# Optimization experiments

Measured on AMD Instinct MI355X. Metric: run time of the kernel, lower is better.

Reference implementation:

```python
import jax, jax.numpy as jnp
import numpy as np

NUM_HEADS = 8


def setup_inputs() -> dict:
    key = jax.random.key(0)
    ks = jax.random.split(key, 8)
    B, N, D, H = 4, 1200, 256, NUM_HEADS
    return {
        "query_bbox": jax.random.normal(ks[0], (B, N, 10), jnp.float32) * 20.0,
        "query_feat": jax.random.normal(ks[1], (B, N, D), jnp.float32),
        "beta_w": jax.random.normal(ks[2], (H, D), jnp.float32) * 0.02,
        "beta_b": jax.random.uniform(ks[3], (H,), jnp.float32, 0.0, 2.0),
        "in_proj_w": jax.random.normal(ks[4], (3 * D, D), jnp.float32) * (D ** -0.5),
        "in_proj_b": jnp.zeros((3 * D,), jnp.float32),
        "out_proj_w": jax.random.normal(ks[5], (D, D), jnp.float32) * (D ** -0.5),
        "out_proj_b": jnp.zeros((D,), jnp.float32),
    }


def reference(query_bbox, query_feat, beta_w, beta_b, in_proj_w, in_proj_b,
              out_proj_w, out_proj_b):
    B, N, D = query_feat.shape
    H = NUM_HEADS
    hd = D // H

    # center_dists (no_grad in original): negative pairwise L2 of bbox centers
    centers = jax.lax.stop_gradient(query_bbox[..., :2])            # [B,N,2]
    diff = centers[:, :, None, :] - centers[:, None, :, :]          # [B,N,N,2]
    dist = -jnp.sqrt(jnp.sum(diff * diff, axis=-1))                 # [B,N,N]

    # per-head learned beta scale
    beta = jnp.einsum('bnd,hd->bhn', query_feat, beta_w) + beta_b[None, :, None]  # [B,H,N]
    attn_mask = dist[:, None, :, :] * beta[..., None]               # [B,H,N,N]

    # multi-head self-attention with additive mask
    qkv = jnp.einsum('bnd,ed->bne', query_feat, in_proj_w) + in_proj_b
    q, k, v = jnp.split(qkv, 3, axis=-1)
    q = q.reshape(B, N, H, hd)
    k = k.reshape(B, N, H, hd)
    v = v.reshape(B, N, H, hd)

    scores = jnp.einsum('bqhd,bkhd->bhqk', q, k) * (hd ** -0.5) + attn_mask
    attn = jax.nn.softmax(scores, axis=-1)                          # [B,H,N,N]
    out = jnp.einsum('bhqk,bkhd->bqhd', attn, v).reshape(B, N, D)
    return jnp.einsum('bnd,ed->bne', out, out_proj_w) + out_proj_b
```

## Files before the change

kernel.cpp:

```cpp
#include <hip/hip_runtime.h>
#include <hip/hip_bf16.h>

#define BC 4
#define NQ 1200
#define DIM 256
#define NH 8
#define HD 32
#define E3 768
#define MROWS (BC*NQ)
#define KPAD 1280
#define SCALE 0.17677669529663687f
#define L2E 1.4426950408889634f
#define SL2E (SCALE * L2E)

#define VT2_PER_BH 40960
#define VT2_PER_HH 20480

typedef __attribute__((ext_vector_type(8))) short bf16x8;
typedef __attribute__((ext_vector_type(4))) float f32x4;

__device__ inline short f2bf(float f) {
    __hip_bfloat16 h = __float2bfloat16(f);
    return *reinterpret_cast<short*>(&h);
}
__device__ inline unsigned pack2bf(float a, float b) {
    unsigned ua = (unsigned short)f2bf(a);
    unsigned ub = (unsigned short)f2bf(b);
    return ua | (ub << 16);
}

__global__ void beta_ctr_kernel(const float* __restrict__ feat, const float* __restrict__ bw,
                                const float* __restrict__ bb, const float* __restrict__ bbox,
                                float* __restrict__ beta, float* __restrict__ ctr) {
    int gw = (blockIdx.x * 256 + threadIdx.x) >> 6;
    int lane = threadIdx.x & 63;
    if (gw >= MROWS) return;
    const float* frow = feat + (size_t)gw * DIM;
    float acc[NH];
#pragma unroll
    for (int h = 0; h < NH; ++h) acc[h] = 0.f;
#pragma unroll
    for (int it = 0; it < DIM / 64; ++it) {
        int d = it * 64 + lane;
        float f = frow[d];
#pragma unroll
        for (int h = 0; h < NH; ++h) acc[h] += f * bw[h * DIM + d];
    }
#pragma unroll
    for (int h = 0; h < NH; ++h) {
#pragma unroll
        for (int off = 32; off; off >>= 1) acc[h] += __shfl_xor(acc[h], off);
    }
    int b = gw / NQ, n = gw % NQ;
#pragma unroll
    for (int h = 0; h < NH; ++h) {
        float v = acc[h] + bb[h];
        if (lane == h) beta[(b * NH + h) * NQ + n] = v;
    }
    if (lane == 0) {
        ctr[gw * 2]     = bbox[(size_t)gw * 10];
        ctr[gw * 2 + 1] = bbox[(size_t)gw * 10 + 1];
    }
}

template<bool AF32, bool BF32, bool OUTF32, bool VTOUT, bool QSCALE>
__global__ __launch_bounds__(256) void gemm_k256(const void* __restrict__ Av,
                                                 const void* __restrict__ Bv,
                                                 const float* __restrict__ bias,
                                                 void* __restrict__ Cout, int Edim,
                                                 short* __restrict__ vtout) {
    __shared__ short as[64][40];
    __shared__ short bs[64][40];
    int m0 = blockIdx.y * 64, e0 = blockIdx.x * 64;
    int t = threadIdx.x, lane = t & 63, wid = t >> 6;
    int wr = (wid >> 1) * 32, wc = (wid & 1) * 32;
    f32x4 acc[2][2] = {};
    int lrow = t >> 2, lch = t & 3;
    const float qs = (QSCALE && e0 < DIM) ? SL2E : 1.f;

    for (int ks = 0; ks < DIM / 32; ++ks) {
        bf16x8 av, wv;
        if (AF32) {
            const float* A = (const float*)Av;
            float4 f0 = *(const float4*)(A + (size_t)(m0 + lrow) * DIM + ks * 32 + lch * 8);
            float4 f1 = *(const float4*)(A + (size_t)(m0 + lrow) * DIM + ks * 32 + lch * 8 + 4);
            av[0]=f2bf(f0.x); av[1]=f2bf(f0.y); av[2]=f2bf(f0.z); av[3]=f2bf(f0.w);
            av[4]=f2bf(f1.x); av[5]=f2bf(f1.y); av[6]=f2bf(f1.z); av[7]=f2bf(f1.w);
        } else {
            av = *(const bf16x8*)((const short*)Av + (size_t)(m0 + lrow) * DIM + ks * 32 + lch * 8);
        }
        if (BF32) {
            const float* B = (const float*)Bv;
            float4 f0 = *(const float4*)(B + (size_t)(e0 + lrow) * DIM + ks * 32 + lch * 8);
            float4 f1 = *(const float4*)(B + (size_t)(e0 + lrow) * DIM + ks * 32 + lch * 8 + 4);
            wv[0]=f2bf(f0.x*qs); wv[1]=f2bf(f0.y*qs); wv[2]=f2bf(f0.z*qs); wv[3]=f2bf(f0.w*qs);
            wv[4]=f2bf(f1.x*qs); wv[5]=f2bf(f1.y*qs); wv[6]=f2bf(f1.z*qs); wv[7]=f2bf(f1.w*qs);
        } else {
            wv = *(const bf16x8*)((const short*)Bv + (size_t)(e0 + lrow) * DIM + ks * 32 + lch * 8);
        }
        __syncthreads();
        *(bf16x8*)&as[lrow][lch * 8] = av;
        *(bf16x8*)&bs[lrow][lch * 8] = wv;
        __syncthreads();
#pragma unroll
        for (int sm = 0; sm < 2; ++sm) {
            bf16x8 af = *(const bf16x8*)&as[wr + sm * 16 + (lane & 15)][(lane >> 4) * 8];
#pragma unroll
            for (int sn = 0; sn < 2; ++sn) {
                bf16x8 bfv = *(const bf16x8*)&bs[wc + sn * 16 + (lane & 15)][(lane >> 4) * 8];
                acc[sm][sn] = __builtin_amdgcn_mfma_f32_16x16x32_bf16(af, bfv, acc[sm][sn], 0, 0, 0);
            }
        }
    }
#pragma unroll
    for (int sm = 0; sm < 2; ++sm)
#pragma unroll
        for (int sn = 0; sn < 2; ++sn) {
            int e = e0 + wc + sn * 16 + (lane & 15);
            float bv = bias[e];
            if (QSCALE && e < DIM) bv *= SL2E;
            float vals[4];
            int mbase = m0 + wr + sm * 16 + (lane >> 4) * 4;
#pragma unroll
            for (int r = 0; r < 4; ++r) vals[r] = acc[sm][sn][r] + bv;
            if (VTOUT && e >= 2 * DIM) {
                int dv = e - 2 * DIM;
                int hv = dv >> 5, dd = dv & 31;
                int hh = dd >> 4, di = dd & 15;
                int bb = mbase / NQ, nn = mbase - bb * NQ;
                short4 o;
                o.x = f2bf(vals[0]); o.y = f2bf(vals[1]);
                o.z = f2bf(vals[2]); o.w = f2bf(vals[3]);
                size_t off = (size_t)(bb * NH + hv) * VT2_PER_BH + hh * VT2_PER_HH
                           + (nn >> 3) * 128 + di * 8 + (nn & 7);
                *(short4*)&vtout[off] = o;
            } else {
#pragma unroll
                for (int r = 0; r < 4; ++r) {
                    int m = mbase + r;
                    if (OUTF32) ((float*)Cout)[(size_t)m * Edim + e] = vals[r];
                    else        ((short*)Cout)[(size_t)m * Edim + e] = f2bf(vals[r]);
                }
            }
        }
}

#define KT_OFF 0
#define VT_OFF 8192
#define CK_OFF 16384
#define PL_OFF 17408
__global__ __launch_bounds__(256, 4) void attn_kernel(const short* __restrict__ qkv,
                                                      const short* __restrict__ vt2,
                                                      const float* __restrict__ beta,
                                                      const float* __restrict__ ctr,
                                                      short* __restrict__ attnb) {
    __shared__ __align__(16) char smem[25600];

    const int t = threadIdx.x, lane = t & 63, w = t >> 6;
    const int g = lane >> 4, i = lane & 15;
    const int qg = w >> 1, ksp = w & 1;
    const int bh = blockIdx.y, b = bh >> 3, h = bh & 7;
    const int q0 = blockIdx.x * 32 + qg * 16;
    const int q = q0 + i, qc = min(q, NQ - 1);
    const int kwb = ksp * 64;
    const int bq = b * NQ;

    bf16x8 qf = *(const bf16x8*)(qkv + (size_t)(bq + qc) * E3 + h * HD + g * 8);
    const float cqx = ctr[(bq + qc) * 2];
    const float cqy = ctr[(bq + qc) * 2 + 1];
    const float nbql = -beta[(b * NH + h) * NQ + qc] * L2E;

    float mcur = -1e30f, lsum = 0.f;
    f32x4 o0 = {}, o1 = {};

    const short* kgb = qkv + (size_t)bq * E3 + DIM + h * HD;
    const short* vgb = vt2 + (size_t)bh * VT2_PER_BH;
    const float* cgb = ctr + (size_t)bq * 2;

    bf16x8 sk0, sk1, sv0, sv1;
    float2 sc2;

    auto stage_load = [&](int kb) {
        int i0 = t, i1 = t + 256;
        int r0 = min(kb + ((i0 >> 6) << 4) + (i0 & 15), NQ - 1);
        int r1 = min(kb + ((i1 >> 6) << 4) + (i1 & 15), NQ - 1);
        sk0 = *(const bf16x8*)(kgb + (size_t)r0 * E3 + ((i0 >> 4) & 3) * 8);
        sk1 = *(const bf16x8*)(kgb + (size_t)r1 * E3 + ((i1 >> 4) & 3) * 8);
        sv0 = *(const bf16x8*)(vgb + (i0 >> 8) * VT2_PER_HH + ((kb >> 3) + ((i0 >> 4) & 15)) * 128 + (i0 & 15) * 8);
        sv1 = *(const bf16x8*)(vgb + (i1 >> 8) * VT2_PER_HH + ((kb >> 3) + ((i1 >> 4) & 15)) * 128 + (i1 & 15) * 8);
        if (t < 128) {
            int ky = min(kb + t, NQ - 1);
            sc2 = *(const float2*)(cgb + ky * 2);
        }
    };
    auto stage_write = [&]() {
        *(bf16x8*)&smem[KT_OFF + t * 16]         = sk0;
        *(bf16x8*)&smem[KT_OFF + (t + 256) * 16] = sk1;
        *(bf16x8*)&smem[VT_OFF + t * 16]         = sv0;
        *(bf16x8*)&smem[VT_OFF + (t + 256) * 16] = sv1;
        if (t < 128) *(float2*)&smem[CK_OFF + t * 8] = sc2;
    };

    stage_load(0);
    stage_write();
    __syncthreads();

    for (int kb = 0; kb < NQ; kb += 128) {
        const bool haveNext = (kb + 128 < NQ);
        const bool tail = (kb + 128 > NQ);
        if (haveNext) stage_load(kb + 128);

        float st[16];
#pragma unroll
        for (int kcl = 0; kcl < 4; ++kcl) {
            bf16x8 af = *(const bf16x8*)&smem[KT_OFF + ((((ksp * 4 + kcl) << 6) + lane) << 4)];
            f32x4 zero = {};
            f32x4 s = __builtin_amdgcn_mfma_f32_16x16x32_bf16(af, qf, zero, 0, 0, 0);
            int lk = kwb + kcl * 16 + 4 * g;
            float4 cA = *(const float4*)&smem[CK_OFF + lk * 8];
            float4 cB = *(const float4*)&smem[CK_OFF + lk * 8 + 16];
            float cxv[4] = {cA.x, cA.z, cB.x, cB.z};
            float cyv[4] = {cA.y, cA.w, cB.y, cB.w};
#pragma unroll
            for (int r = 0; r < 4; ++r) {
                float dx = cqx - cxv[r], dy = cqy - cyv[r];
                float d2 = __builtin_fmaf(dx, dx, dy * dy);
                float dist = __builtin_amdgcn_sqrtf(d2);
                st[kcl * 4 + r] = __builtin_fmaf(dist, nbql, s[r]);
            }
            if (tail) {
#pragma unroll
                for (int r = 0; r < 4; ++r)
                    if (kb + lk + r >= NQ) st[kcl * 4 + r] = -1e30f;
            }
        }

        float vm = st[0];
#pragma unroll
        for (int x = 1; x < 16; ++x) vm = fmaxf(vm, st[x]);
        vm = fmaxf(vm, __shfl_xor(vm, 16));
        vm = fmaxf(vm, __shfl_xor(vm, 32));
        if (!__all(vm <= mcur + 8.0f)) {
            float mnew = fmaxf(mcur, vm);
            float al = __builtin_amdgcn_exp2f(mcur - mnew);
            mcur = mnew;
            lsum *= al;
#pragma unroll
            for (int r = 0; r < 4; ++r) { o0[r] *= al; o1[r] *= al; }
        }
        float rs = 0.f;
#pragma unroll
        for (int x = 0; x < 16; ++x) {
            st[x] = __builtin_amdgcn_exp2f(st[x] - mcur);
            rs += st[x];
        }
        rs += __shfl_xor(rs, 16);
        rs += __shfl_xor(rs, 32);
        lsum += rs;

#pragma unroll
        for (int kcl = 0; kcl < 4; ++kcl) {
            int offb = PL_OFF + (((w << 10) + ((2 * kcl + (g >> 1)) << 7) + (i << 3) + ((g & 1) << 2)) << 1);
            *(unsigned*)&smem[offb]     = pack2bf(st[kcl * 4 + 0], st[kcl * 4 + 1]);
            *(unsigned*)&smem[offb + 4] = pack2bf(st[kcl * 4 + 2], st[kcl * 4 + 3]);
        }

#pragma unroll
        for (int kc2 = 0; kc2 < 2; ++kc2) {
            bf16x8 pbf = *(const bf16x8*)&smem[PL_OFF + (((w << 10) + ((kc2 * 4 + g) << 7) + (i << 3)) << 1)];
            int vidx = ((8 * ksp + 4 * kc2 + g) << 4) + i;
            bf16x8 vf0 = *(const bf16x8*)&smem[VT_OFF + (vidx << 4)];
            bf16x8 vf1 = *(const bf16x8*)&smem[VT_OFF + ((256 + vidx) << 4)];
            o0 = __builtin_amdgcn_mfma_f32_16x16x32_bf16(vf0, pbf, o0, 0, 0, 0);
            o1 = __builtin_amdgcn_mfma_f32_16x16x32_bf16(vf1, pbf, o1, 0, 0, 0);
        }

        if (haveNext) {
            __syncthreads();
            stage_write();
            __syncthreads();
        }
    }

    __syncthreads();
    float* mrg = (float*)smem;
    float* my = mrg + (w * 64 + lane) * 10;
    my[0] = mcur; my[1] = lsum;
#pragma unroll
    for (int r = 0; r < 4; ++r) { my[2 + r] = o0[r]; my[6 + r] = o1[r]; }
    __syncthreads();
    const float* pr = mrg + ((w ^ 1) * 64 + lane) * 10;
    float m2 = pr[0], l2 = pr[1];
    float mN = fmaxf(mcur, m2);
    float a1 = __builtin_amdgcn_exp2f(mcur - mN);
    float a2 = __builtin_amdgcn_exp2f(m2 - mN);
    float inv = 1.f / (lsum * a1 + l2 * a2);
    int hh = w & 1;
    f32x4 mine = hh ? o1 : o0;
    if (q < NQ) {
        short4 outv;
        float vals[4];
#pragma unroll
        for (int r = 0; r < 4; ++r) vals[r] = (mine[r] * a1 + pr[2 + hh * 4 + r] * a2) * inv;
        outv.x = f2bf(vals[0]); outv.y = f2bf(vals[1]);
        outv.z = f2bf(vals[2]); outv.w = f2bf(vals[3]);
        *(short4*)&attnb[(size_t)(bq + q) * DIM + h * HD + hh * 16 + 4 * g] = outv;
    }
}

extern "C" void kernel_launch(void* const* d_in, const int* in_sizes, int n_in,
                              void* d_out, int out_size, void* d_ws, size_t ws_size,
                              hipStream_t stream) {
    const float* bbox  = (const float*)d_in[0];
    const float* feat  = (const float*)d_in[1];
    const float* bw    = (const float*)d_in[2];
    const float* bb    = (const float*)d_in[3];
    const float* in_w  = (const float*)d_in[4];
    const float* in_b  = (const float*)d_in[5];
    const float* out_w = (const float*)d_in[6];
    const float* out_b = (const float*)d_in[7];
    float* out = (float*)d_out;

    char* ws = (char*)d_ws;
    size_t off = 0;
    auto alloc = [&](size_t bytes) { void* p = ws + off; off += (bytes + 255) & ~255ull; return p; };
    short* qkvb  = (short*)alloc((size_t)MROWS * E3 * 2);
    short* vtb   = (short*)alloc((size_t)BC * NH * VT2_PER_BH * 2);
    short* attnb = (short*)alloc((size_t)MROWS * DIM * 2);
    float* betab = (float*)alloc((size_t)BC * NH * NQ * 4);
    float* ctr   = (float*)alloc((size_t)BC * NQ * 2 * 4 + 1024);
    (void)ws_size; (void)in_sizes; (void)n_in; (void)out_size;

    beta_ctr_kernel<<<MROWS / 4, 256, 0, stream>>>(feat, bw, bb, bbox, betab, ctr);
    gemm_k256<true, true, false, true, true><<<dim3(E3 / 64, MROWS / 64), 256, 0, stream>>>(feat, in_w, in_b, qkvb, E3, vtb);
    attn_kernel<<<dim3((NQ + 31) / 32, BC * NH), 256, 0, stream>>>(qkvb, vtb, betab, ctr, attnb);
    gemm_k256<false, true, true, false, false><<<dim3(DIM / 64, MROWS / 64), 256, 0, stream>>>(attnb, out_w, out_b, out, DIM, nullptr);
}
```

Baseline: 59.96 us.

## Split each attention block's key range across four waves with 16 queries per block

The attention kernel now handles 16 queries per block instead of 32, and the four waves split each 128-key tile into four 32-key slices rather than two query groups times two key halves. The final merge combines four partial softmax states. This doubles the grid to 75x32 blocks, cuts per-thread register and LDS use, and raises launch bounds to 6 blocks per CU for more occupancy. In exchange, each block loads K/V tiles for fewer queries, so global and LDS traffic per query doubles, and the merge step does more work.

Result: slower. 67.31 us (+12.3%).

```diff
diff --git a/kernel.cpp b/kernel.cpp
--- a/kernel.cpp
+++ b/kernel.cpp
@@ -8,7 +8,6 @@
 #define HD 32
 #define E3 768
 #define MROWS (BC*NQ)
-#define KPAD 1280
 #define SCALE 0.17677669529663687f
 #define L2E 1.4426950408889634f
 #define SL2E (SCALE * L2E)
@@ -149,26 +148,25 @@
 #define VT_OFF 8192
 #define CK_OFF 16384
 #define PL_OFF 17408
-__global__ __launch_bounds__(256, 4) void attn_kernel(const short* __restrict__ qkv,
+__global__ __launch_bounds__(256, 6) void attn_kernel(const short* __restrict__ qkv,
                                                       const short* __restrict__ vt2,
                                                       const float* __restrict__ beta,
                                                       const float* __restrict__ ctr,
                                                       short* __restrict__ attnb) {
-    __shared__ __align__(16) char smem[25600];
+    __shared__ __align__(16) char smem[21504];
 
     const int t = threadIdx.x, lane = t & 63, w = t >> 6;
     const int g = lane >> 4, i = lane & 15;
-    const int qg = w >> 1, ksp = w & 1;
+    const int ksp = w;
     const int bh = blockIdx.y, b = bh >> 3, h = bh & 7;
-    const int q0 = blockIdx.x * 32 + qg * 16;
-    const int q = q0 + i, qc = min(q, NQ - 1);
-    const int kwb = ksp * 64;
+    const int q = blockIdx.x * 16 + i;
+    const int kwb = ksp * 32;
     const int bq = b * NQ;
 
-    bf16x8 qf = *(const bf16x8*)(qkv + (size_t)(bq + qc) * E3 + h * HD + g * 8);
-    const float cqx = ctr[(bq + qc) * 2];
-    const float cqy = ctr[(bq + qc) * 2 + 1];
-    const float nbql = -beta[(b * NH + h) * NQ + qc] * L2E;
+    bf16x8 qf = *(const bf16x8*)(qkv + (size_t)(bq + q) * E3 + h * HD + g * 8);
+    const float cqx = ctr[(bq + q) * 2];
+    const float cqy = ctr[(bq + q) * 2 + 1];
+    const float nbql = -beta[(b * NH + h) * NQ + q] * L2E;
 
     float mcur = -1e30f, lsum = 0.f;
     f32x4 o0 = {}, o1 = {};
@@ -210,10 +208,10 @@
         const bool tail = (kb + 128 > NQ);
         if (haveNext) stage_load(kb + 128);
 
-        float st[16];
-#pragma unroll
-        for (int kcl = 0; kcl < 4; ++kcl) {
-            bf16x8 af = *(const bf16x8*)&smem[KT_OFF + ((((ksp * 4 + kcl) << 6) + lane) << 4)];
+        float st[8];
+#pragma unroll
+        for (int kcl = 0; kcl < 2; ++kcl) {
+            bf16x8 af = *(const bf16x8*)&smem[KT_OFF + ((((ksp * 2 + kcl) << 6) + lane) << 4)];
             f32x4 zero = {};
             f32x4 s = __builtin_amdgcn_mfma_f32_16x16x32_bf16(af, qf, zero, 0, 0, 0);
             int lk = kwb + kcl * 16 + 4 * g;
@@ -235,9 +233,9 @@
             }
         }
 
-        float vm = st[0];
-#pragma unroll
-        for (int x = 1; x < 16; ++x) vm = fmaxf(vm, st[x]);
+        float m01 = fmaxf(st[0], st[1]), m23 = fmaxf(st[2], st[3]);
+        float m45 = fmaxf(st[4], st[5]), m67 = fmaxf(st[6], st[7]);
+        float vm = fmaxf(fmaxf(m01, m23), fmaxf(m45, m67));
         vm = fmaxf(vm, __shfl_xor(vm, 16));
         vm = fmaxf(vm, __shfl_xor(vm, 32));
         if (!__all(vm <= mcur + 8.0f)) {
@@ -248,29 +246,25 @@
 #pragma unroll
             for (int r = 0; r < 4; ++r) { o0[r] *= al; o1[r] *= al; }
         }
-        float rs = 0.f;
-#pragma unroll
-        for (int x = 0; x < 16; ++x) {
-            st[x] = __builtin_amdgcn_exp2f(st[x] - mcur);
-            rs += st[x];
-        }
+#pragma unroll
+        for (int x = 0; x < 8; ++x) st[x] = __builtin_amdgcn_exp2f(st[x] - mcur);
+        float rs = ((st[0] + st[1]) + (st[2] + st[3])) + ((st[4] + st[5]) + (st[6] + st[7]));
         rs += __shfl_xor(rs, 16);
         rs += __shfl_xor(rs, 32);
         lsum += rs;
 
 #pragma unroll
-        for (int kcl = 0; kcl < 4; ++kcl) {
-            int offb = PL_OFF + (((w << 10) + ((2 * kcl + (g >> 1)) << 7) + (i << 3) + ((g & 1) << 2)) << 1);
+        for (int kcl = 0; kcl < 2; ++kcl) {
+            int offb = PL_OFF + (w << 10) + ((2 * kcl + (g >> 1)) << 8) + (i << 4) + ((g & 1) << 3);
             *(unsigned*)&smem[offb]     = pack2bf(st[kcl * 4 + 0], st[kcl * 4 + 1]);
             *(unsigned*)&smem[offb + 4] = pack2bf(st[kcl * 4 + 2], st[kcl * 4 + 3]);
         }
 
-#pragma unroll
-        for (int kc2 = 0; kc2 < 2; ++kc2) {
-            bf16x8 pbf = *(const bf16x8*)&smem[PL_OFF + (((w << 10) + ((kc2 * 4 + g) << 7) + (i << 3)) << 1)];
-            int vidx = ((8 * ksp + 4 * kc2 + g) << 4) + i;
+        {
+            bf16x8 pbf = *(const bf16x8*)&smem[PL_OFF + (w << 10) + (g << 8) + (i << 4)];
+            int vidx = (((ksp << 2) + g) << 4) + i;
             bf16x8 vf0 = *(const bf16x8*)&smem[VT_OFF + (vidx << 4)];
-            bf16x8 vf1 = *(const bf16x8*)&smem[VT_OFF + ((256 + vidx) << 4)];
+            bf16x8 vf1 = *(const bf16x8*)&smem[VT_OFF + 4096 + (vidx << 4)];
             o0 = __builtin_amdgcn_mfma_f32_16x16x32_bf16(vf0, pbf, o0, 0, 0, 0);
             o1 = __builtin_amdgcn_mfma_f32_16x16x32_bf16(vf1, pbf, o1, 0, 0, 0);
         }
@@ -289,19 +283,25 @@
 #pragma unroll
     for (int r = 0; r < 4; ++r) { my[2 + r] = o0[r]; my[6 + r] = o1[r]; }
     __syncthreads();
-    const float* pr = mrg + ((w ^ 1) * 64 + lane) * 10;
-    float m2 = pr[0], l2 = pr[1];
-    float mN = fmaxf(mcur, m2);
-    float a1 = __builtin_amdgcn_exp2f(mcur - mN);
-    float a2 = __builtin_amdgcn_exp2f(m2 - mN);
-    float inv = 1.f / (lsum * a1 + l2 * a2);
-    int hh = w & 1;
-    f32x4 mine = hh ? o1 : o0;
-    if (q < NQ) {
+    if (w < 2) {
+        const float* p0 = mrg + lane * 10;
+        const float* p1 = mrg + (64 + lane) * 10;
+        const float* p2 = mrg + (128 + lane) * 10;
+        const float* p3 = mrg + (192 + lane) * 10;
+        float mN = fmaxf(fmaxf(p0[0], p1[0]), fmaxf(p2[0], p3[0]));
+        float a0 = __builtin_amdgcn_exp2f(p0[0] - mN);
+        float a1 = __builtin_amdgcn_exp2f(p1[0] - mN);
+        float a2 = __builtin_amdgcn_exp2f(p2[0] - mN);
+        float a3 = __builtin_amdgcn_exp2f(p3[0] - mN);
+        float inv = 1.f / (p0[1] * a0 + p1[1] * a1 + p2[1] * a2 + p3[1] * a3);
+        int hh = w;
         short4 outv;
         float vals[4];
 #pragma unroll
-        for (int r = 0; r < 4; ++r) vals[r] = (mine[r] * a1 + pr[2 + hh * 4 + r] * a2) * inv;
+        for (int r = 0; r < 4; ++r) {
+            int o = 2 + hh * 4 + r;
+            vals[r] = (p0[o] * a0 + p1[o] * a1 + p2[o] * a2 + p3[o] * a3) * inv;
+        }
         outv.x = f2bf(vals[0]); outv.y = f2bf(vals[1]);
         outv.z = f2bf(vals[2]); outv.w = f2bf(vals[3]);
         *(short4*)&attnb[(size_t)(bq + q) * DIM + h * HD + hh * 16 + 4 * g] = outv;
@@ -333,6 +333,6 @@
 
     beta_ctr_kernel<<<MROWS / 4, 256, 0, stream>>>(feat, bw, bb, bbox, betab, ctr);
     gemm_k256<true, true, false, true, true><<<dim3(E3 / 64, MROWS / 64), 256, 0, stream>>>(feat, in_w, in_b, qkvb, E3, vtb);
-    attn_kernel<<<dim3((NQ + 31) / 32, BC * NH), 256, 0, stream>>>(qkvb, vtb, betab, ctr, attnb);
+    attn_kernel<<<dim3(75, BC * NH), 256, 0, stream>>>(qkvb, vtb, betab, ctr, attnb);
     gemm_k256<false, true, true, false, false><<<dim3(DIM / 64, MROWS / 64), 256, 0, stream>>>(attnb, out_w, out_b, out, DIM, nullptr);
 }
```

## Double-buffer K/V tiles in LDS and fold running max into MFMA accumulator

Applied to the files above, without the earlier changes.

Switches the attention kernel's K/V/center staging to a double-buffered LDS layout, so each iteration needs one barrier instead of two. The running max is now subtracted by initialising the QK MFMA accumulator with -mcur, which removes the per-element subtraction before exp2. Global load pointers are precomputed and advanced incrementally, and the P tile staging is shrunk to a per-half reuse. The max and sum reductions are also made tree-shaped. The cost is roughly 13 KB more LDS per block, which may lower occupancy under launch_bounds(256,4). The pointer changes also drop the clamp on tail rows, so the last tile can read past row NQ-1.

Result: no change. 60.73 us (+1.3%).

```diff
diff --git a/kernel.cpp b/kernel.cpp
--- a/kernel.cpp
+++ b/kernel.cpp
@@ -8,7 +8,6 @@
 #define HD 32
 #define E3 768
 #define MROWS (BC*NQ)
-#define KPAD 1280
 #define SCALE 0.17677669529663687f
 #define L2E 1.4426950408889634f
 #define SL2E (SCALE * L2E)
@@ -18,6 +17,7 @@
 
 typedef __attribute__((ext_vector_type(8))) short bf16x8;
 typedef __attribute__((ext_vector_type(4))) float f32x4;
+typedef __attribute__((ext_vector_type(2))) unsigned u32x2;
 
 __device__ inline short f2bf(float f) {
     __hip_bfloat16 h = __float2bfloat16(f);
@@ -145,16 +145,17 @@
         }
 }
 
+#define BUFSZ 17408
 #define KT_OFF 0
 #define VT_OFF 8192
 #define CK_OFF 16384
-#define PL_OFF 17408
+#define PL_OFF (2*BUFSZ)
 __global__ __launch_bounds__(256, 4) void attn_kernel(const short* __restrict__ qkv,
                                                       const short* __restrict__ vt2,
                                                       const float* __restrict__ beta,
                                                       const float* __restrict__ ctr,
                                                       short* __restrict__ attnb) {
-    __shared__ __align__(16) char smem[25600];
+    __shared__ __align__(16) char smem[2 * BUFSZ + 4096];
 
     const int t = threadIdx.x, lane = t & 63, w = t >> 6;
     const int g = lane >> 4, i = lane & 15;
@@ -170,55 +171,55 @@
     const float cqy = ctr[(bq + qc) * 2 + 1];
     const float nbql = -beta[(b * NH + h) * NQ + qc] * L2E;
 
-    float mcur = -1e30f, lsum = 0.f;
+    float mcur = 0.f, lsum = 0.f;
     f32x4 o0 = {}, o1 = {};
 
-    const short* kgb = qkv + (size_t)bq * E3 + DIM + h * HD;
-    const short* vgb = vt2 + (size_t)bh * VT2_PER_BH;
-    const float* cgb = ctr + (size_t)bq * 2;
+    const int koff = ((t >> 6) << 4) + (t & 15);
+    const short* kld0 = qkv + (size_t)bq * E3 + DIM + h * HD + (size_t)koff * E3 + ((t >> 4) & 3) * 8;
+    const short* kld1 = kld0 + (size_t)64 * E3;
+    const short* vld0 = vt2 + (size_t)bh * VT2_PER_BH + (((t >> 4) & 15)) * 128 + (t & 15) * 8;
+    const short* vld1 = vld0 + VT2_PER_HH;
+    const float* cld = ctr + (size_t)bq * 2 + t * 2;
 
     bf16x8 sk0, sk1, sv0, sv1;
     float2 sc2;
-
-    auto stage_load = [&](int kb) {
-        int i0 = t, i1 = t + 256;
-        int r0 = min(kb + ((i0 >> 6) << 4) + (i0 & 15), NQ - 1);
-        int r1 = min(kb + ((i1 >> 6) << 4) + (i1 & 15), NQ - 1);
-        sk0 = *(const bf16x8*)(kgb + (size_t)r0 * E3 + ((i0 >> 4) & 3) * 8);
-        sk1 = *(const bf16x8*)(kgb + (size_t)r1 * E3 + ((i1 >> 4) & 3) * 8);
-        sv0 = *(const bf16x8*)(vgb + (i0 >> 8) * VT2_PER_HH + ((kb >> 3) + ((i0 >> 4) & 15)) * 128 + (i0 & 15) * 8);
-        sv1 = *(const bf16x8*)(vgb + (i1 >> 8) * VT2_PER_HH + ((kb >> 3) + ((i1 >> 4) & 15)) * 128 + (i1 & 15) * 8);
-        if (t < 128) {
-            int ky = min(kb + t, NQ - 1);
-            sc2 = *(const float2*)(cgb + ky * 2);
-        }
+    auto stage_load = [&]() {
+        sk0 = *(const bf16x8*)kld0;
+        sk1 = *(const bf16x8*)kld1;
+        sv0 = *(const bf16x8*)vld0;
+        sv1 = *(const bf16x8*)vld1;
+        if (t < 128) sc2 = *(const float2*)cld;
+        kld0 += (size_t)128 * E3; kld1 += (size_t)128 * E3;
+        vld0 += 2048; vld1 += 2048; cld += 256;
     };
-    auto stage_write = [&]() {
-        *(bf16x8*)&smem[KT_OFF + t * 16]         = sk0;
-        *(bf16x8*)&smem[KT_OFF + (t + 256) * 16] = sk1;
-        *(bf16x8*)&smem[VT_OFF + t * 16]         = sv0;
-        *(bf16x8*)&smem[VT_OFF + (t + 256) * 16] = sv1;
-        if (t < 128) *(float2*)&smem[CK_OFF + t * 8] = sc2;
+    auto stage_write = [&](int base) {
+        *(bf16x8*)&smem[base + KT_OFF + t * 16]         = sk0;
+        *(bf16x8*)&smem[base + KT_OFF + (t + 256) * 16] = sk1;
+        *(bf16x8*)&smem[base + VT_OFF + t * 16]         = sv0;
+        *(bf16x8*)&smem[base + VT_OFF + (t + 256) * 16] = sv1;
+        if (t < 128) *(float2*)&smem[base + CK_OFF + t * 8] = sc2;
     };
 
-    stage_load(0);
-    stage_write();
+    stage_load();
+    stage_write(0);
     __syncthreads();
+    int cur = 0;
 
     for (int kb = 0; kb < NQ; kb += 128) {
         const bool haveNext = (kb + 128 < NQ);
         const bool tail = (kb + 128 > NQ);
-        if (haveNext) stage_load(kb + 128);
-
+        if (haveNext) stage_load();
+
+        const int cb = cur * BUFSZ;
         float st[16];
+        f32x4 cinit = {-mcur, -mcur, -mcur, -mcur};
 #pragma unroll
         for (int kcl = 0; kcl < 4; ++kcl) {
-            bf16x8 af = *(const bf16x8*)&smem[KT_OFF + ((((ksp * 4 + kcl) << 6) + lane) << 4)];
-            f32x4 zero = {};
-            f32x4 s = __builtin_amdgcn_mfma_f32_16x16x32_bf16(af, qf, zero, 0, 0, 0);
+            bf16x8 af = *(const bf16x8*)&smem[cb + KT_OFF + (((ksp * 4 + kcl) * 64 + lane) << 4)];
+            f32x4 s = __builtin_amdgcn_mfma_f32_16x16x32_bf16(af, qf, cinit, 0, 0, 0);
             int lk = kwb + kcl * 16 + 4 * g;
-            float4 cA = *(const float4*)&smem[CK_OFF + lk * 8];
-            float4 cB = *(const float4*)&smem[CK_OFF + lk * 8 + 16];
+            float4 cA = *(const float4*)&smem[cb + CK_OFF + lk * 8];
+            float4 cB = *(const float4*)&smem[cb + CK_OFF + lk * 8 + 16];
             float cxv[4] = {cA.x, cA.z, cB.x, cB.z};
             float cyv[4] = {cA.y, cA.w, cB.y, cB.w};
 #pragma unroll
@@ -235,54 +236,57 @@
             }
         }
 
-        float vm = st[0];
-#pragma unroll
-        for (int x = 1; x < 16; ++x) vm = fmaxf(vm, st[x]);
+        float a0 = fmaxf(fmaxf(st[0],  st[1]),  st[2]);
+        float a1 = fmaxf(fmaxf(st[3],  st[4]),  st[5]);
+        float a2 = fmaxf(fmaxf(st[6],  st[7]),  st[8]);
+        float a3 = fmaxf(fmaxf(st[9],  st[10]), st[11]);
+        float a4 = fmaxf(fmaxf(st[12], st[13]), st[14]);
+        float vm = fmaxf(fmaxf(fmaxf(a0, a1), a2), fmaxf(fmaxf(a3, a4), st[15]));
         vm = fmaxf(vm, __shfl_xor(vm, 16));
         vm = fmaxf(vm, __shfl_xor(vm, 32));
-        if (!__all(vm <= mcur + 8.0f)) {
-            float mnew = fmaxf(mcur, vm);
-            float al = __builtin_amdgcn_exp2f(mcur - mnew);
-            mcur = mnew;
+        if (!__all(vm <= 8.0f)) {
+            float dm = fmaxf(vm, 0.f);
+            float al = __builtin_amdgcn_exp2f(-dm);
+            mcur += dm;
             lsum *= al;
 #pragma unroll
             for (int r = 0; r < 4; ++r) { o0[r] *= al; o1[r] *= al; }
-        }
-        float rs = 0.f;
-#pragma unroll
-        for (int x = 0; x < 16; ++x) {
-            st[x] = __builtin_amdgcn_exp2f(st[x] - mcur);
-            rs += st[x];
-        }
+#pragma unroll
+            for (int x = 0; x < 16; ++x) st[x] -= dm;
+        }
+#pragma unroll
+        for (int x = 0; x < 16; ++x) st[x] = __builtin_amdgcn_exp2f(st[x]);
+        float s0 = (st[0] + st[1]) + (st[2] + st[3]);
+        float s1 = (st[4] + st[5]) + (st[6] + st[7]);
+        float s2 = (st[8] + st[9]) + (st[10] + st[11]);
+        float s3 = (st[12] + st[13]) + (st[14] + st[15]);
+        float rs = (s0 + s1) + (s2 + s3);
         rs += __shfl_xor(rs, 16);
         rs += __shfl_xor(rs, 32);
         lsum += rs;
 
 #pragma unroll
-        for (int kcl = 0; kcl < 4; ++kcl) {
-            int offb = PL_OFF + (((w << 10) + ((2 * kcl + (g >> 1)) << 7) + (i << 3) + ((g & 1) << 2)) << 1);
-            *(unsigned*)&smem[offb]     = pack2bf(st[kcl * 4 + 0], st[kcl * 4 + 1]);
-            *(unsigned*)&smem[offb + 4] = pack2bf(st[kcl * 4 + 2], st[kcl * 4 + 3]);
-        }
-
-#pragma unroll
         for (int kc2 = 0; kc2 < 2; ++kc2) {
-            bf16x8 pbf = *(const bf16x8*)&smem[PL_OFF + (((w << 10) + ((kc2 * 4 + g) << 7) + (i << 3)) << 1)];
-            int vidx = ((8 * ksp + 4 * kc2 + g) << 4) + i;
-            bf16x8 vf0 = *(const bf16x8*)&smem[VT_OFF + (vidx << 4)];
-            bf16x8 vf1 = *(const bf16x8*)&smem[VT_OFF + ((256 + vidx) << 4)];
+#pragma unroll
+            for (int kk = 0; kk < 2; ++kk) {
+                int kcl = 2 * kc2 + kk;
+                u32x2 pw = {pack2bf(st[kcl * 4 + 0], st[kcl * 4 + 1]),
+                            pack2bf(st[kcl * 4 + 2], st[kcl * 4 + 3])};
+                *(u32x2*)&smem[PL_OFF + (w << 10) + (((kk << 1) + (g >> 1)) << 8) + (i << 4) + ((g & 1) << 3)] = pw;
+            }
+            bf16x8 pbf = *(const bf16x8*)&smem[PL_OFF + (w << 10) + (g << 8) + (i << 4)];
+            int vidx = (8 * ksp + 4 * kc2 + g) * 16 + i;
+            bf16x8 vf0 = *(const bf16x8*)&smem[cb + VT_OFF + (vidx << 4)];
+            bf16x8 vf1 = *(const bf16x8*)&smem[cb + VT_OFF + ((256 + vidx) << 4)];
             o0 = __builtin_amdgcn_mfma_f32_16x16x32_bf16(vf0, pbf, o0, 0, 0, 0);
             o1 = __builtin_amdgcn_mfma_f32_16x16x32_bf16(vf1, pbf, o1, 0, 0, 0);
         }
 
-        if (haveNext) {
-            __syncthreads();
-            stage_write();
-            __syncthreads();
-        }
-    }
-
-    __syncthreads();
+        if (haveNext) stage_write((cur ^ 1) * BUFSZ);
+        __syncthreads();
+        cur ^= 1;
+    }
+
     float* mrg = (float*)smem;
     float* my = mrg + (w * 64 + lane) * 10;
     my[0] = mcur; my[1] = lsum;
```
